# Kernel tuning notes

Measured on AMD Instinct MI355X. Metric: run time of the kernel, lower is better.

Reference implementation:

```python
import jax, jax.numpy as jnp
import numpy as np

B, C, H, W = 16, 64, 128, 128
C8 = C // 8

def setup_inputs() -> dict:
    key = jax.random.key(0)
    ks = jax.random.split(key, 9)
    s = 0.05
    return {
        "x": jax.random.normal(ks[0], (B, C, H, W), jnp.float32),
        "y": jax.random.normal(ks[1], (B, C, H, W), jnp.float32),
        "query_w": jax.random.normal(ks[2], (C8, C), jnp.float32) * s,
        "query_b": jax.random.normal(ks[3], (C8,), jnp.float32) * s,
        "key_w": jax.random.normal(ks[4], (C8, C), jnp.float32) * s,
        "key_b": jax.random.normal(ks[5], (C8,), jnp.float32) * s,
        "value_w": jax.random.normal(ks[6], (C, 2 * C), jnp.float32) * s,
        "value_b": jax.random.normal(ks[7], (C,), jnp.float32) * s,
        "gamma": jax.random.normal(ks[8], (), jnp.float32) * 0.1,
    }

def _conv1x1(t, w, b):
    # t: [B, Cin, H, W], w: [Cout, Cin] -> [B, Cout, H, W]
    return jnp.einsum('oc,bchw->bohw', w, t) + b[None, :, None, None]

def reference(x, y, query_w, query_b, key_w, key_b, value_w, value_b, gamma):
    b, c, h, w = x.shape
    q = _conv1x1(x, query_w, query_b)                       # [B, C8, H, W]
    k = _conv1x1(y, key_w, key_b)                           # [B, C8, H, W]
    v = _conv1x1(jnp.concatenate([x, y], axis=1), value_w, value_b)  # [B, C, H, W]

    # axial energies: H-axis (g indexes key rows), W-axis (u indexes key cols)
    energy_H = jnp.einsum('bchw,bcgw->bhwg', q, k)          # [B, H, W, H]
    energy_W = jnp.einsum('bchw,bchu->bhwu', q, k)          # [B, H, W, W]

    # -inf on the H diagonal (self position counted once, via the W branch)
    eye = jnp.eye(h, dtype=bool)                            # [H, H]
    energy_H = jnp.where(eye[None, :, None, :], -jnp.inf, energy_H)

    att = jax.nn.softmax(jnp.concatenate([energy_H, energy_W], axis=3), axis=3)
    att_H = att[..., :h]                                    # [B, H, W, H]
    att_W = att[..., h:]                                    # [B, H, W, W]

    out_H = jnp.einsum('bcgw,bhwg->bchw', v, att_H)
    out_W = jnp.einsum('bchu,bhwu->bchw', v, att_W)
    return gamma * (out_H + out_W) + x + y
```

## Files before the change

kernel.cpp:

```cpp
#include <hip/hip_runtime.h>

#define NCH 80
#define HW 16384

typedef unsigned short u16;
typedef unsigned int u32;
typedef short s16x8 __attribute__((ext_vector_type(8)));
typedef float f32x4 __attribute__((ext_vector_type(4)));

__device__ __forceinline__ float b2f_lo(u32 pk){ union{u32 u; float f;} c; c.u = pk<<16; return c.f; }
__device__ __forceinline__ float b2f_hi(u32 pk){ union{u32 u; float f;} c; c.u = pk & 0xffff0000u; return c.f; }
__device__ __forceinline__ u16 f2b_hw(float f){
    union{ __bf16 h; u16 s; } c; c.h = (__bf16)f; return c.s;
}
__device__ __forceinline__ u32 pk2(float a, float b){
    return (u32)f2b_hw(a) | ((u32)f2b_hw(b)<<16);
}
#define NEG_INF (-__builtin_inff())

union U4S8 { uint4 u; s16x8 v; };

__device__ __forceinline__ int swz_px(int cin, int px){
    int q = cin >> 3;
    return px ^ ((q & 3) << 2) ^ ((q & 1) << 4);
}

__device__ __forceinline__ void gload_lds16(const void* g, void* l){
    __builtin_amdgcn_global_load_lds(
        (const __attribute__((address_space(1))) void*)g,
        (__attribute__((address_space(3))) void*)l,
        16, 0, 0);
}

__global__ __launch_bounds__(256) void k_wcvt(
    const float* __restrict__ qw, const float* __restrict__ qb,
    const float* __restrict__ kw, const float* __restrict__ kb,
    const float* __restrict__ vw, const float* __restrict__ vb,
    u16* __restrict__ wbf, float* __restrict__ bias80)
{
    int i = blockIdx.x*256 + threadIdx.x;
    int ch = i >> 7, cin = i & 127;
    float v;
    if (ch < 8)       v = (cin < 64) ? qw[ch*64 + cin] : 0.f;
    else if (ch < 16) v = (cin >= 64) ? kw[(ch-8)*64 + (cin-64)] : 0.f;
    else              v = vw[(ch-16)*128 + cin];
    wbf[i] = f2b_hw(v);
    if (i < 80){
        bias80[i] = (i<8) ? qb[i] : (i<16) ? kb[i-8] : vb[i-16];
    }
}

__global__ __launch_bounds__(256) void k_qkv_mfma(
    const float* __restrict__ x, const float* __restrict__ y,
    const u16* __restrict__ wbf, const float* __restrict__ bias80,
    u16* __restrict__ qkv, u16* __restrict__ xy)
{
    __shared__ float xs_lds[128*64];

    int t = threadIdx.x;
    int wv = t >> 6, l = t & 63;
    int p0 = blockIdx.x * 64;
    int b = p0 >> 14, rem = p0 & 16383;

    const float* xb = x + (size_t)b*64*HW + rem;
    const float* yb = y + (size_t)b*64*HW + rem;

    #pragma unroll
    for (int i=0;i<8;i++){
        int s = wv*8 + i;
        int cin = s*4 + (l>>4);
        int pxg = swz_px(cin, (l&15)*4);
        const float* gp = (cin < 64) ? (xb + (size_t)cin*HW + pxg)
                                     : (yb + (size_t)(cin-64)*HW + pxg);
        gload_lds16(gp, (char*)xs_lds + s*1024);
    }
    __syncthreads();

    int lm = l & 15, lq = l >> 4;
    int px = wv*16 + lm;

    s16x8 af[4];
    #pragma unroll
    for (int ks=0; ks<4; ks++){
        float fv[8];
        #pragma unroll
        for (int j=0;j<8;j++){
            int cin = ks*32 + lq*8 + j;
            fv[j] = xs_lds[cin*64 + swz_px(cin, px)];
        }
        U4S8 uu;
        uu.u = make_uint4(pk2(fv[0],fv[1]), pk2(fv[2],fv[3]),
                          pk2(fv[4],fv[5]), pk2(fv[6],fv[7]));
        af[ks] = uu.v;
    }

    #pragma unroll
    for (int nt=0;nt<5;nt++){
        int ch = nt*16 + lm;
        const u16* wrow = wbf + ch*128 + lq*8;
        f32x4 acc = (f32x4){0.f,0.f,0.f,0.f};
        #pragma unroll
        for (int ks=0;ks<4;ks++){
            s16x8 bfrag = *(const s16x8*)(wrow + ks*32);
            acc = __builtin_amdgcn_mfma_f32_16x16x32_bf16(af[ks], bfrag, acc, 0,0,0);
        }
        float bs = bias80[ch];
        uint2 st;
        st.x = pk2(acc[0]+bs, acc[1]+bs);
        st.y = pk2(acc[2]+bs, acc[3]+bs);
        *(uint2*)&qkv[(size_t)(b*NCH + ch)*HW + rem + wv*16 + lq*4] = st;
    }

    if (xy){
        u32* xyp = (u32*)xy;
        #pragma unroll
        for (int r=0;r<8;r++){
            int oi = t + r*256;
            int ch = oi >> 5;
            int pxp = oi & 31;
            int wx = ch*64 + swz_px(ch, 2*pxp);
            int wyi = (ch+64)*64 + swz_px(ch+64, 2*pxp);
            float2 xv = *(float2*)&xs_lds[wx];
            float2 yv = *(float2*)&xs_lds[wyi];
            xyp[((size_t)(b*64+ch)*HW + rem)/2 + pxp] = pk2(xv.x+yv.x, xv.y+yv.y);
        }
    }
}

__global__ __launch_bounds__(256) void k_tr(const u16* __restrict__ src, u16* __restrict__ dst)
{
    __shared__ u16 tile[64][65];
    int blk = blockIdx.x;
    int plane = blk >> 2, tq = blk & 3;
    int r0 = (tq >> 1) * 64, c0 = (tq & 1) * 64;
    const u16* s = src + (size_t)plane * HW;
    u16* d = dst + (size_t)plane * HW;
    int col = threadIdx.x & 63, rr = threadIdx.x >> 6;
    #pragma unroll
    for (int k=0;k<16;k++){
        int r = k*4 + rr;
        tile[r][col] = s[(r0+r)*128 + c0 + col];
    }
    __syncthreads();
    #pragma unroll
    for (int k=0;k<16;k++){
        int r = k*4 + rr;
        d[(c0+r)*128 + r0 + col] = tile[col][r];
    }
}

__global__ __launch_bounds__(512, 4) void k_col(
    const u16* __restrict__ qkvT, u16* __restrict__ colT,
    float* __restrict__ mH, float* __restrict__ sH)
{
    __shared__ __align__(16) float q_s[8*128];
    __shared__ __align__(16) float k_sw[8*128];
    __shared__ __align__(16) u16  v_bf[64*128];
    __shared__ __align__(16) u16  p_bf[128*128];

    int t = threadIdx.x;
    int b = blockIdx.x >> 7, w = blockIdx.x & 127;
    const u32* src = (const u32*)(qkvT + (size_t)b*NCH*HW + w*128);
    u32* v32 = (u32*)v_bf;
    u32* p32 = (u32*)p_bf;

    #pragma unroll
    for (int r=0;r<2;r++){
        int idx = t + r*512;
        int ch = idx >> 6, hp = idx & 63;
        u32 pk = src[ch*8192 + hp];
        int g0 = hp*2;
        if (ch < 8){
            *(float2*)&q_s[ch*128 + g0] = make_float2(b2f_lo(pk), b2f_hi(pk));
        } else {
            int o = ch - 8;
            k_sw[g0*8     + (o ^ ((g0>>3)&7))]     = b2f_lo(pk);
            k_sw[(g0+1)*8 + (o ^ (((g0+1)>>3)&7))] = b2f_hi(pk);
        }
    }
    #pragma unroll
    for (int r=0;r<8;r++){
        int idx = t + r*512;
        int c = idx >> 6, gp = idx & 63;
        v32[(c*64 + gp) ^ ((c&7)<<2)] = src[(16+c)*8192 + gp];
    }
    __syncthreads();

    int tr = t >> 4, tc = t & 15;
    int h0 = tr*4, g0 = tc*8;
    float e[4][8];
    #pragma unroll
    for (int i=0;i<4;i++)
        #pragma unroll
        for (int j=0;j<8;j++) e[i][j] = 0.f;

    #pragma unroll
    for (int o=0;o<8;o++){
        float qv[4], kv[8];
        #pragma unroll
        for (int i=0;i<4;i++) qv[i] = q_s[o*128 + h0 + i];
        int kb = o ^ (tc & 7);
        #pragma unroll
        for (int j=0;j<8;j++) kv[j] = k_sw[(g0+j)*8 + kb];
        #pragma unroll
        for (int i=0;i<4;i++)
            #pragma unroll
            for (int j=0;j<8;j++) e[i][j] += qv[i]*kv[j];
    }
    #pragma unroll
    for (int i=0;i<4;i++){
        int h = h0 + i;
        if ((h>>3) == tc) e[i][h&7] = NEG_INF;
    }
    #pragma unroll
    for (int i=0;i<4;i++){
        int h = h0 + i;
        float m = e[i][0];
        #pragma unroll
        for (int j=1;j<8;j++) m = fmaxf(m, e[i][j]);
        m = fmaxf(m, __shfl_xor(m,1));
        m = fmaxf(m, __shfl_xor(m,2));
        m = fmaxf(m, __shfl_xor(m,4));
        m = fmaxf(m, __shfl_xor(m,8));
        float s = 0.f;
        #pragma unroll
        for (int j=0;j<8;j++){ float pp = __expf(e[i][j]-m); e[i][j]=pp; s += pp; }
        s += __shfl_xor(s,1);
        s += __shfl_xor(s,2);
        s += __shfl_xor(s,4);
        s += __shfl_xor(s,8);
        if (tc == 0){
            mH[b*HW + h*128 + w] = m;
            sH[b*HW + h*128 + w] = s;
        }
        uint4 pw;
        pw.x = pk2(e[i][0], e[i][1]);
        pw.y = pk2(e[i][2], e[i][3]);
        pw.z = pk2(e[i][4], e[i][5]);
        pw.w = pk2(e[i][6], e[i][7]);
        *(uint4*)&p32[(h*64 + tc*4) ^ ((h&7)<<2)] = pw;
    }
    __syncthreads();

    int wv = t >> 6, l = t & 63;
    int lm = l & 15, lq = l >> 4;
    int mt = wv;
    f32x4 acc[4];
    #pragma unroll
    for (int nt=0; nt<4; nt++) acc[nt] = (f32x4){0.f,0.f,0.f,0.f};

    #pragma unroll
    for (int ks=0; ks<4; ks++){
        int ri = mt*16 + lm;
        s16x8 a = *(const s16x8*)&p32[(ri*64 + ks*16 + lq*4) ^ ((ri&7)<<2)];
        #pragma unroll
        for (int nt=0; nt<4; nt++){
            int c = nt*16 + lm;
            s16x8 bf_ = *(const s16x8*)&v32[(c*64 + ks*16 + lq*4) ^ ((c&7)<<2)];
            acc[nt] = __builtin_amdgcn_mfma_f32_16x16x32_bf16(a, bf_, acc[nt], 0, 0, 0);
        }
    }
    #pragma unroll
    for (int nt=0; nt<4; nt++){
        int c = nt*16 + lm;
        int hh = mt*16 + lq*4;
        uint2 st;
        st.x = pk2(acc[nt][0], acc[nt][1]);
        st.y = pk2(acc[nt][2], acc[nt][3]);
        *(uint2*)&colT[((size_t)(b*64+c)*128 + w)*128 + hh] = st;
    }
}

__global__ __launch_bounds__(512, 4) void k_row(
    const u16* __restrict__ qkv, const u16* __restrict__ colpart,
    const float* __restrict__ mH, const float* __restrict__ sH,
    const float* __restrict__ x, const float* __restrict__ y,
    const u16* __restrict__ xy,
    const float* __restrict__ gamma_p, float* __restrict__ out)
{
    __shared__ __align__(16) float q_s[8*128];
    __shared__ __align__(16) float k_sw[8*128];
    __shared__ __align__(16) u16  v_bf[64*128];
    __shared__ __align__(16) u16  p_bf[128*128];
    __shared__ float fc_s[128], fr_s[128];

    int t = threadIdx.x;
    int b = blockIdx.x >> 7, h = blockIdx.x & 127;
    const u32* src = (const u32*)(qkv + (size_t)b*NCH*HW + h*128);
    u32* v32 = (u32*)v_bf;
    u32* p32 = (u32*)p_bf;

    #pragma unroll
    for (int r=0;r<2;r++){
        int idx = t + r*512;
        int ch = idx >> 6, wp = idx & 63;
        u32 pk = src[ch*8192 + wp];
        int u0 = wp*2;
        if (ch < 8){
            *(float2*)&q_s[ch*128 + u0] = make_float2(b2f_lo(pk), b2f_hi(pk));
        } else {
            int o = ch - 8;
            k_sw[u0*8     + (o ^ ((u0>>3)&7))]     = b2f_lo(pk);
            k_sw[(u0+1)*8 + (o ^ (((u0+1)>>3)&7))] = b2f_hi(pk);
        }
    }
    #pragma unroll
    for (int r=0;r<8;r++){
        int idx = t + r*512;
        int c = idx >> 6, up = idx & 63;
        v32[(c*64 + up) ^ ((c&7)<<2)] = src[(16+c)*8192 + up];
    }
    __syncthreads();

    int tr = t >> 4, tc = t & 15;
    int w0 = tr*4, u0 = tc*8;
    float e[4][8];
    #pragma unroll
    for (int i=0;i<4;i++)
        #pragma unroll
        for (int j=0;j<8;j++) e[i][j] = 0.f;

    #pragma unroll
    for (int o=0;o<8;o++){
        float qv[4], kv[8];
        #pragma unroll
        for (int i=0;i<4;i++) qv[i] = q_s[o*128 + w0 + i];
        int kb = o ^ (tc & 7);
        #pragma unroll
        for (int j=0;j<8;j++) kv[j] = k_sw[(u0+j)*8 + kb];
        #pragma unroll
        for (int i=0;i<4;i++)
            #pragma unroll
            for (int j=0;j<8;j++) e[i][j] += qv[i]*kv[j];
    }
    int pixbase = b*HW + h*128;
    #pragma unroll
    for (int i=0;i<4;i++){
        int wp = w0 + i;
        float m = e[i][0];
        #pragma unroll
        for (int j=1;j<8;j++) m = fmaxf(m, e[i][j]);
        m = fmaxf(m, __shfl_xor(m,1));
        m = fmaxf(m, __shfl_xor(m,2));
        m = fmaxf(m, __shfl_xor(m,4));
        m = fmaxf(m, __shfl_xor(m,8));
        float mh = mH[pixbase + wp];
        float sh = sH[pixbase + wp];
        float mg = fmaxf(m, mh);
        float s = 0.f;
        #pragma unroll
        for (int j=0;j<8;j++){ float pp = __expf(e[i][j]-mg); e[i][j]=pp; s += pp; }
        s += __shfl_xor(s,1);
        s += __shfl_xor(s,2);
        s += __shfl_xor(s,4);
        s += __shfl_xor(s,8);
        if (tc == 0){
            float ef = __expf(mh - mg);
            float stot = sh*ef + s;
            fc_s[wp] = ef/stot;
            fr_s[wp] = 1.0f/stot;
        }
        uint4 pw;
        pw.x = pk2(e[i][0], e[i][1]);
        pw.y = pk2(e[i][2], e[i][3]);
        pw.z = pk2(e[i][4], e[i][5]);
        pw.w = pk2(e[i][6], e[i][7]);
        *(uint4*)&p32[(wp*64 + tc*4) ^ ((wp&7)<<2)] = pw;
    }
    __syncthreads();

    int wv = t >> 6, l = t & 63;
    int lm = l & 15, lq = l >> 4;
    int mt = wv;
    f32x4 acc[4];
    #pragma unroll
    for (int nt=0; nt<4; nt++) acc[nt] = (f32x4){0.f,0.f,0.f,0.f};

    #pragma unroll
    for (int ks=0; ks<4; ks++){
        int ri = mt*16 + lm;
        s16x8 a = *(const s16x8*)&p32[(ri*64 + ks*16 + lq*4) ^ ((ri&7)<<2)];
        #pragma unroll
        for (int nt=0; nt<4; nt++){
            int c = nt*16 + lm;
            s16x8 bf_ = *(const s16x8*)&v32[(c*64 + ks*16 + lq*4) ^ ((c&7)<<2)];
            acc[nt] = __builtin_amdgcn_mfma_f32_16x16x32_bf16(a, bf_, acc[nt], 0, 0, 0);
        }
    }
    float gm = gamma_p[0];
    int wq0 = mt*16 + lq*4;
    float fcv[4], frv[4];
    #pragma unroll
    for (int r2=0;r2<4;r2++){ fcv[r2] = fc_s[wq0+r2]; frv[r2] = fr_s[wq0+r2]; }

    #pragma unroll
    for (int nt=0; nt<4; nt++){
        int c = nt*16 + lm;
        size_t off = ((size_t)(b*64+c)*128 + h)*128 + wq0;
        uint2 cpv = *(const uint2*)&colpart[off];
        float cp[4] = {b2f_lo(cpv.x), b2f_hi(cpv.x), b2f_lo(cpv.y), b2f_hi(cpv.y)};
        float xs[4];
        if (xy){
            uint2 xv = *(const uint2*)&xy[off];
            xs[0]=b2f_lo(xv.x); xs[1]=b2f_hi(xv.x); xs[2]=b2f_lo(xv.y); xs[3]=b2f_hi(xv.y);
        } else {
            float4 x4 = *(const float4*)&x[off];
            float4 y4 = *(const float4*)&y[off];
            xs[0]=x4.x+y4.x; xs[1]=x4.y+y4.y; xs[2]=x4.z+y4.z; xs[3]=x4.w+y4.w;
        }
        float4 o4;
        o4.x = gm*(cp[0]*fcv[0] + acc[nt][0]*frv[0]) + xs[0];
        o4.y = gm*(cp[1]*fcv[1] + acc[nt][1]*frv[1]) + xs[1];
        o4.z = gm*(cp[2]*fcv[2] + acc[nt][2]*frv[2]) + xs[2];
        o4.w = gm*(cp[3]*fcv[3] + acc[nt][3]*frv[3]) + xs[3];
        *(float4*)&out[off] = o4;
    }
}

extern "C" void kernel_launch(void* const* d_in, const int* in_sizes, int n_in,
                              void* d_out, int out_size, void* d_ws, size_t ws_size,
                              hipStream_t stream)
{
    (void)in_sizes; (void)n_in; (void)out_size;
    const float* x  = (const float*)d_in[0];
    const float* y  = (const float*)d_in[1];
    const float* qw = (const float*)d_in[2];
    const float* qb = (const float*)d_in[3];
    const float* kw = (const float*)d_in[4];
    const float* kb = (const float*)d_in[5];
    const float* vw = (const float*)d_in[6];
    const float* vb = (const float*)d_in[7];
    const float* gm = (const float*)d_in[8];
    float* out = (float*)d_out;

    char* ws = (char*)d_ws;
    u16* qkv     = (u16*)(ws);
    u16* qkvT    = (u16*)(ws + 41943040ull);
    u16* colT    = (u16*)(ws + 83886080ull);
    u16* colpart = qkvT;
    float* mH    = (float*)(ws + 117440512ull);
    float* sH    = (float*)(ws + 118489088ull);
    u16* wbf     = (u16*)(ws + 119537664ull);
    float* bias80= (float*)(ws + 119558144ull);
    u16* xybuf   = nullptr;
    if (ws_size >= 119603200ull + 33554432ull)
        xybuf = (u16*)(ws + 119603200ull);

    k_wcvt<<<40, 256, 0, stream>>>(qw, qb, kw, kb, vw, vb, wbf, bias80);
    k_qkv_mfma<<<4096, 256, 0, stream>>>(x, y, wbf, bias80, qkv, xybuf);
    k_tr <<<5120, 256, 0, stream>>>(qkv, qkvT);
    k_col<<<2048, 512, 0, stream>>>(qkvT, colT, mH, sH);
    k_tr <<<4096, 256, 0, stream>>>(colT, colpart);
    k_row<<<2048, 512, 0, stream>>>(qkv, colpart, mH, sH, x, y, xybuf, gm, out);
}
```

Baseline: 187.5 us.

## Restructure QKV projection into double-buffered K-pipelined tiles of 512 pixels

Each QKV 1x1-conv block now covers 512 pixels with 512 threads, not 64 pixels. The K dimension is split into four stages of 16 x-channels plus 16 y-channels, streamed into a double-buffered LDS tile so that global-to-LDS loads overlap the MFMA work. The weight layout is permuted to match the interleaved channel stages, and the x+y sum is written per stage. The goal is fewer blocks, reuse of the weight fragments across four pixel tiles, and hidden load latency, at the cost of 128KB of LDS per block and lower occupancy.

Result: faster. 176.2 us (-6.0%).

```diff
diff --git a/kernel.cpp b/kernel.cpp
--- a/kernel.cpp
+++ b/kernel.cpp
@@ -20,9 +20,8 @@
 
 union U4S8 { uint4 u; s16x8 v; };
 
-__device__ __forceinline__ int swz_px(int cin, int px){
-    int q = cin >> 3;
-    return px ^ ((q & 3) << 2) ^ ((q & 1) << 4);
+__device__ __forceinline__ int swz_row(int r){
+    return ((r & 7) << 2) ^ ((r & 8) << 1);
 }
 
 __device__ __forceinline__ void gload_lds16(const void* g, void* l){
@@ -39,7 +38,9 @@
     u16* __restrict__ wbf, float* __restrict__ bias80)
 {
     int i = blockIdx.x*256 + threadIdx.x;
-    int ch = i >> 7, cin = i & 127;
+    int ch = i >> 7, k = i & 127;
+    int s = k >> 5, j = k & 31;
+    int cin = (j < 16) ? (s*16 + j) : (64 + s*16 + (j - 16));
     float v;
     if (ch < 8)       v = (cin < 64) ? qw[ch*64 + cin] : 0.f;
     else if (ch < 16) v = (cin >= 64) ? kw[(ch-8)*64 + (cin-64)] : 0.f;
@@ -50,79 +51,102 @@
     }
 }
 
-__global__ __launch_bounds__(256) void k_qkv_mfma(
+__global__ __launch_bounds__(512) void k_qkv_mfma(
     const float* __restrict__ x, const float* __restrict__ y,
     const u16* __restrict__ wbf, const float* __restrict__ bias80,
     u16* __restrict__ qkv, u16* __restrict__ xy)
 {
-    __shared__ float xs_lds[128*64];
+    __shared__ float buf[2][32*512];
 
     int t = threadIdx.x;
     int wv = t >> 6, l = t & 63;
-    int p0 = blockIdx.x * 64;
+    int lm = l & 15, lq = l >> 4;
+    int p0 = blockIdx.x * 512;
     int b = p0 >> 14, rem = p0 & 16383;
-
     const float* xb = x + (size_t)b*64*HW + rem;
     const float* yb = y + (size_t)b*64*HW + rem;
+    u32* xyp = (u32*)xy;
+
+    f32x4 acc[4][5];
+    #pragma unroll
+    for (int mi=0;mi<4;mi++)
+        #pragma unroll
+        for (int nt=0;nt<5;nt++) acc[mi][nt] = (f32x4){0.f,0.f,0.f,0.f};
 
     #pragma unroll
     for (int i=0;i<8;i++){
-        int s = wv*8 + i;
-        int cin = s*4 + (l>>4);
-        int pxg = swz_px(cin, (l&15)*4);
-        const float* gp = (cin < 64) ? (xb + (size_t)cin*HW + pxg)
-                                     : (yb + (size_t)(cin-64)*HW + pxg);
-        gload_lds16(gp, (char*)xs_lds + s*1024);
-    }
-    __syncthreads();
-
-    int lm = l & 15, lq = l >> 4;
-    int px = wv*16 + lm;
-
-    s16x8 af[4];
-    #pragma unroll
-    for (int ks=0; ks<4; ks++){
-        float fv[8];
-        #pragma unroll
-        for (int j=0;j<8;j++){
-            int cin = ks*32 + lq*8 + j;
-            fv[j] = xs_lds[cin*64 + swz_px(cin, px)];
-        }
-        U4S8 uu;
-        uu.u = make_uint4(pk2(fv[0],fv[1]), pk2(fv[2],fv[3]),
-                          pk2(fv[4],fv[5]), pk2(fv[6],fv[7]));
-        af[ks] = uu.v;
-    }
-
-    #pragma unroll
-    for (int nt=0;nt<5;nt++){
-        int ch = nt*16 + lm;
-        const u16* wrow = wbf + ch*128 + lq*8;
-        f32x4 acc = (f32x4){0.f,0.f,0.f,0.f};
-        #pragma unroll
-        for (int ks=0;ks<4;ks++){
-            s16x8 bfrag = *(const s16x8*)(wrow + ks*32);
-            acc = __builtin_amdgcn_mfma_f32_16x16x32_bf16(af[ks], bfrag, acc, 0,0,0);
-        }
-        float bs = bias80[ch];
-        uint2 st;
-        st.x = pk2(acc[0]+bs, acc[1]+bs);
-        st.y = pk2(acc[2]+bs, acc[3]+bs);
-        *(uint2*)&qkv[(size_t)(b*NCH + ch)*HW + rem + wv*16 + lq*4] = st;
-    }
-
-    if (xy){
-        u32* xyp = (u32*)xy;
-        #pragma unroll
-        for (int r=0;r<8;r++){
-            int oi = t + r*256;
-            int ch = oi >> 5;
-            int pxp = oi & 31;
-            int wx = ch*64 + swz_px(ch, 2*pxp);
-            int wyi = (ch+64)*64 + swz_px(ch+64, 2*pxp);
-            float2 xv = *(float2*)&xs_lds[wx];
-            float2 yv = *(float2*)&xs_lds[wyi];
-            xyp[((size_t)(b*64+ch)*HW + rem)/2 + pxp] = pk2(xv.x+yv.x, xv.y+yv.y);
+        int r  = wv*4 + (i>>1);
+        int hh = i & 1;
+        int pxg = (hh*256 + l*4) ^ swz_row(r);
+        const float* gp = (r < 16) ? (xb + (size_t)(r)*HW + pxg)
+                                   : (yb + (size_t)(r-16)*HW + pxg);
+        gload_lds16(gp, (char*)&buf[0][0] + (size_t)(r*512 + hh*256)*4);
+    }
+    __syncthreads();
+
+    #pragma unroll
+    for (int s=0; s<4; s++){
+        int bi = s & 1;
+        if (s < 3){
+            #pragma unroll
+            for (int i=0;i<8;i++){
+                int r  = wv*4 + (i>>1);
+                int hh = i & 1;
+                int pxg = (hh*256 + l*4) ^ swz_row(r);
+                const float* gp = (r < 16) ? (xb + (size_t)((s+1)*16 + r)*HW + pxg)
+                                           : (yb + (size_t)((s+1)*16 + (r-16))*HW + pxg);
+                gload_lds16(gp, (char*)&buf[bi^1][0] + (size_t)(r*512 + hh*256)*4);
+            }
+        }
+        __builtin_amdgcn_sched_barrier(0);
+
+        s16x8 bfr[5];
+        #pragma unroll
+        for (int nt=0;nt<5;nt++)
+            bfr[nt] = *(const s16x8*)(wbf + (nt*16 + lm)*128 + s*32 + lq*8);
+
+        #pragma unroll
+        for (int mi=0;mi<4;mi++){
+            int pxl = (wv*4 + mi)*16 + lm;
+            float fv[8];
+            #pragma unroll
+            for (int jj=0;jj<8;jj++){
+                int r = lq*8 + jj;
+                fv[jj] = buf[bi][r*512 + (pxl ^ swz_row(r))];
+            }
+            U4S8 uu;
+            uu.u = make_uint4(pk2(fv[0],fv[1]), pk2(fv[2],fv[3]),
+                              pk2(fv[4],fv[5]), pk2(fv[6],fv[7]));
+            #pragma unroll
+            for (int nt=0;nt<5;nt++)
+                acc[mi][nt] = __builtin_amdgcn_mfma_f32_16x16x32_bf16(uu.v, bfr[nt], acc[mi][nt], 0,0,0);
+        }
+
+        if (xy){
+            #pragma unroll
+            for (int it=0; it<8; it++){
+                int oi = t + it*512;
+                int j  = oi >> 8;
+                int pp = oi & 255;
+                int sw = swz_row(j);
+                float2 xv = *(float2*)&buf[bi][j*512 + ((2*pp) ^ sw)];
+                float2 yv = *(float2*)&buf[bi][(j+16)*512 + ((2*pp) ^ sw)];
+                xyp[((size_t)(b*64 + s*16 + j)*HW + rem)/2 + pp] = pk2(xv.x+yv.x, xv.y+yv.y);
+            }
+        }
+        __syncthreads();
+    }
+
+    #pragma unroll
+    for (int mi=0;mi<4;mi++){
+        #pragma unroll
+        for (int nt=0;nt<5;nt++){
+            int ch = nt*16 + lm;
+            float bs = bias80[ch];
+            uint2 st;
+            st.x = pk2(acc[mi][nt][0]+bs, acc[mi][nt][1]+bs);
+            st.y = pk2(acc[mi][nt][2]+bs, acc[mi][nt][3]+bs);
+            *(uint2*)&qkv[(size_t)(b*NCH + ch)*HW + rem + (wv*4 + mi)*16 + lq*4] = st;
         }
     }
 }
@@ -447,7 +471,7 @@
         xybuf = (u16*)(ws + 119603200ull);
 
     k_wcvt<<<40, 256, 0, stream>>>(qw, qb, kw, kb, vw, vb, wbf, bias80);
-    k_qkv_mfma<<<4096, 256, 0, stream>>>(x, y, wbf, bias80, qkv, xybuf);
+    k_qkv_mfma<<<512, 512, 0, stream>>>(x, y, wbf, bias80, qkv, xybuf);
     k_tr <<<5120, 256, 0, stream>>>(qkv, qkvT);
     k_col<<<2048, 512, 0, stream>>>(qkvT, colT, mH, sH);
     k_tr <<<4096, 256, 0, stream>>>(colT, colpart);
```
